# Kernel tuning notes

Hardware: AMD Instinct MI355X
Metric: run time of the kernel (lower is better)

Reference implementation:

```python
import jax, jax.numpy as jnp
import numpy as np

B, NPOS, NNEG, D, NLEM = 8, 512, 512, 128, 32768
MOMENTUM = 0.5
EPS = 1e-12  # F.normalize eps


def setup_inputs() -> dict:
    key = jax.random.key(0)
    k1, k2, k3, k4 = jax.random.split(key, 4)
    x = jax.random.normal(k1, (B, NPOS + NNEG, D), dtype=jnp.float32)
    y = jax.random.randint(k2, (B, NPOS), 0, NPOS).astype(jnp.int64)
    visible = jax.random.randint(k3, (B, NPOS), 0, 2).astype(jnp.int32)
    stdv = 1.0 / np.sqrt(D / 3.0)
    memory = jax.random.uniform(k4, (NLEM, D), dtype=jnp.float32,
                                minval=-stdv, maxval=stdv)
    return {"x": x, "y": y, "visible": visible, "memory": memory, "lru": 3}


def reference(x, y, visible, memory, lru):
    # --- similarity computation (differentiable path) ---
    t = x[:, :NPOS, :]                                  # [B, NPOS, D]
    similarity = jnp.einsum('bpd,md->bpm', t, memory)    # [B, NPOS, NLEM]
    noise_similarity = jnp.einsum('bnd,pd->bnp',
                                  x[:, NPOS:, :], memory[:NPOS])  # [B, NNEG, NPOS]
    y_idx = y.astype(jnp.int64)

    # --- memory bank update (no-grad in original) ---
    vis = visible.astype(x.dtype)[..., None]             # [B, NPOS, 1]
    get = jnp.mean(t * vis, axis=0)                      # [NPOS, D]
    pos_new = memory[:NPOS] * MOMENTUM + get * (1.0 - MOMENTUM)
    neg_flat = x[:, NPOS:, :].reshape(-1, D)             # [B*NNEG, D]
    start = NPOS + lru * NNEG * B                        # lru is a python int
    new_mem = memory.at[start:start + NNEG * B].set(neg_flat)
    new_mem = new_mem.at[:NPOS].set(pos_new)
    norms = jnp.maximum(jnp.linalg.norm(new_mem, axis=1, keepdims=True), EPS)
    new_mem = jax.lax.stop_gradient(new_mem / norms)

    return similarity, y_idx, noise_similarity, new_mem
```

## Files before the change

kernel.cpp:

```cpp
#include <hip/hip_runtime.h>
#include <hip/hip_bf16.h>
#include <cstdint>

#define NPOS 512
#define NNEG 512
#define BATCH 8
#define DDIM 128
#define NLEM 32768
#define NX_ELEM (BATCH * (NPOS + NNEG) * DDIM)
#define NM_ELEM (NLEM * DDIM)
#define NK_STEPS 32

typedef __attribute__((ext_vector_type(4))) float f32x4;
typedef __attribute__((ext_vector_type(16))) float f32x16;
typedef __attribute__((ext_vector_type(8))) short short8;

__device__ __forceinline__ unsigned short f2bf(float f) {
  unsigned u = __float_as_uint(f);
  u = (u + 0x7FFFu + ((u >> 16) & 1u)) >> 16;
  return (unsigned short)u;
}

__device__ __forceinline__ short8 cvt8(f32x4 a0, f32x4 a1) {
  short8 w;
  w[0] = (short)f2bf(a0[0]); w[1] = (short)f2bf(a0[1]);
  w[2] = (short)f2bf(a0[2]); w[3] = (short)f2bf(a0[3]);
  w[4] = (short)f2bf(a1[0]); w[5] = (short)f2bf(a1[1]);
  w[6] = (short)f2bf(a1[2]); w[7] = (short)f2bf(a1[3]);
  return w;
}

__device__ __forceinline__ void async16(const void* g, void* l) {
  __builtin_amdgcn_global_load_lds(
      (const __attribute__((address_space(1))) unsigned int*)g,
      (__attribute__((address_space(3))) unsigned int*)l, 16, 0, 0);
}

__device__ __forceinline__ void newmem_row(int r, int lane, const float* __restrict__ X,
                                           const int* __restrict__ vis,
                                           const float* __restrict__ Mem, int start,
                                           float* __restrict__ out) {
  const int d0 = lane, d1 = lane + 64;
  float v0, v1;
  if (r < NPOS) {
    const float s0 = Mem[(size_t)r * DDIM + d0];
    const float s1 = Mem[(size_t)r * DDIM + d1];
    float a0 = 0.f, a1 = 0.f;
#pragma unroll
    for (int b = 0; b < BATCH; ++b) {
      const float w = (float)vis[b * NPOS + r];
      const float* px = X + (size_t)(b * (NPOS + NNEG) + r) * DDIM;
      a0 += w * px[d0];
      a1 += w * px[d1];
    }
    v0 = 0.5f * s0 + 0.0625f * a0;
    v1 = 0.5f * s1 + 0.0625f * a1;
  } else if (r >= start && r < start + BATCH * NNEG) {
    const int q = r - start;
    const int b = q >> 9, n = q & 511;
    const float* px = X + (size_t)(b * (NPOS + NNEG) + NPOS + n) * DDIM;
    v0 = px[d0];
    v1 = px[d1];
  } else {
    v0 = Mem[(size_t)r * DDIM + d0];
    v1 = Mem[(size_t)r * DDIM + d1];
  }
  float s = v0 * v0 + v1 * v1;
#pragma unroll
  for (int off = 32; off; off >>= 1) s += __shfl_xor(s, off, 64);
  const float inv = 1.0f / fmaxf(sqrtf(s), 1e-12f);
  out[(size_t)r * DDIM + d0] = v0 * inv;
  out[(size_t)r * DDIM + d1] = v1 * inv;
}

__global__ __launch_bounds__(256) void prep_kernel(
    const float* __restrict__ X, const int* __restrict__ y,
    const int* __restrict__ vis, const float* __restrict__ Mem,
    const int* __restrict__ lru_p, unsigned short* __restrict__ xb,
    unsigned short* __restrict__ mb, float* __restrict__ out_y,
    float* __restrict__ out_mem) {
  const int blk = blockIdx.x;
  if (blk < 512) {
    const size_t i = ((size_t)blk * 256 + threadIdx.x) * 8;
    *(short8*)(xb + i) = cvt8(*(const f32x4*)(X + i), *(const f32x4*)(X + i + 4));
  } else if (blk < 2560) {
    const size_t i = ((size_t)(blk - 512) * 256 + threadIdx.x) * 8;
    *(short8*)(mb + i) = cvt8(*(const f32x4*)(Mem + i), *(const f32x4*)(Mem + i + 4));
  } else if (blk < 2576) {
    const int i = (blk - 2560) * 256 + threadIdx.x;
    out_y[i] = (float)y[i];
  } else {
    const int r = (blk - 2576) * 4 + (threadIdx.x >> 6);
    const int start = NPOS + lru_p[0] * (NNEG * BATCH);
    newmem_row(r, threadIdx.x & 63, X, vis, Mem, start, out_mem);
  }
}

__device__ __forceinline__ void hoist_b(const short* Btile, short8 bfr[8][2],
                                        int wc, int la, int lb) {
#pragma unroll
  for (int kk = 0; kk < 8; ++kk)
#pragma unroll
    for (int n2 = 0; n2 < 2; ++n2) {
      const int row = wc * 64 + n2 * 32 + la;
      const int ss = ((kk * 2 + lb) ^ (row & 15)) * 8;
      bfr[kk][n2] = *(const short8*)&Btile[row * 128 + ss];
    }
}

__device__ __forceinline__ void tile_mfma(const short* Atile, const short8 bfr[8][2],
                                          f32x16 acc[2][2], int wr, int la, int lb) {
#pragma unroll
  for (int kk = 0; kk < 8; ++kk) {
    short8 af[2];
#pragma unroll
    for (int m2 = 0; m2 < 2; ++m2) {
      const int row = wr * 64 + m2 * 32 + la;
      const int ss = ((kk * 2 + lb) ^ (row & 15)) * 8;
      af[m2] = *(const short8*)&Atile[row * 128 + ss];
    }
#pragma unroll
    for (int m2 = 0; m2 < 2; ++m2)
#pragma unroll
      for (int n2 = 0; n2 < 2; ++n2)
        acc[m2][n2] = __builtin_amdgcn_mfma_f32_32x32x16_bf16(
            af[m2], bfr[kk][n2], acc[m2][n2], 0, 0, 0);
  }
}

__device__ __forceinline__ void epilogue_store(
    float* __restrict__ ldsC, const f32x16 acc[2][2], float* __restrict__ C,
    int ldc, int m0, int n0c, int t, int wr, int wc, int la, int lb) {
  const int rg = t >> 5, l5 = t & 31;
#pragma unroll
  for (int H = 0; H < 2; ++H) {
    if (wr == H) {
#pragma unroll
      for (int m2 = 0; m2 < 2; ++m2)
#pragma unroll
        for (int n2 = 0; n2 < 2; ++n2) {
          const int colb = wc * 64 + n2 * 32 + la;
          const int rb = m2 * 32 + lb * 4;
#pragma unroll
          for (int r = 0; r < 16; ++r) {
            const int rho = rb + (r & 3) + 8 * (r >> 2);
            ldsC[rho * 132 + colb] = acc[m2][n2][r];
          }
        }
    }
    asm volatile("s_waitcnt lgkmcnt(0)" ::: "memory");
    __builtin_amdgcn_s_barrier();
    __builtin_amdgcn_sched_barrier(0);
#pragma unroll
    for (int i = 0; i < 8; ++i) {
      const int rho = rg + 8 * i;
      const f32x4 v = *(const f32x4*)&ldsC[rho * 132 + l5 * 4];
      *(f32x4*)&C[(size_t)(m0 + H * 64 + rho) * ldc + n0c + l5 * 4] = v;
    }
    if (H == 0) {
      __builtin_amdgcn_s_barrier();
      __builtin_amdgcn_sched_barrier(0);
    }
  }
}

__global__ __launch_bounds__(256, 1) void gemm_band_kernel(
    const unsigned short* __restrict__ Xb, const unsigned short* __restrict__ Mb,
    float* __restrict__ Csim, float* __restrict__ Cnoise) {
  __shared__ short ldsA[2][128 * 128];
  __shared__ short ldsB[128 * 128];
  __shared__ float ldsC[64 * 132];

  const int t = threadIdx.x;
  const int lane = t & 63, wv = t >> 6;
  const int rl = lane >> 4, slot = lane & 15;
  const int wr = wv >> 1, wc = wv & 1;
  const int la = lane & 31, lb = lane >> 5;
  const int b = blockIdx.x;
  const int n0 = b * 128;

  auto stage_tile = [&](short* dst, const unsigned short* src, int rowbase) {
#pragma unroll
    for (int i = 0; i < 8; ++i) {
      const int rowb = wv * 32 + i * 4;
      const int row = rowb + rl;
      const int ss = slot ^ (row & 15);
      async16(src + (size_t)(rowbase + row) * DDIM + ss * 8, &dst[rowb * 128]);
    }
  };

  stage_tile(ldsB, Mb, n0);
  stage_tile(ldsA[0], Xb, 0);
  asm volatile("s_waitcnt vmcnt(0)" ::: "memory");
  __builtin_amdgcn_s_barrier();
  __builtin_amdgcn_sched_barrier(0);

  short8 bfr[8][2];
  hoist_b(ldsB, bfr, wc, la, lb);

  int p = 0;
  for (int k = 0; k < NK_STEPS; ++k) {
    if (k + 1 < NK_STEPS) {
      const int kn = k + 1;
      stage_tile(ldsA[p ^ 1], Xb, (kn >> 2) * 1024 + (kn & 3) * 128);
    } else if (b < 128) {
      const int rp = b >> 2, cb = b & 3;
      stage_tile(ldsA[p ^ 1], Xb, (rp >> 2) * 1024 + 512 + (rp & 3) * 128);
      stage_tile(ldsB, Mb, cb * 128);
    }

    f32x16 acc[2][2] = {};
    tile_mfma(ldsA[p], bfr, acc, wr, la, lb);
    epilogue_store(ldsC, acc, Csim, NLEM, k * 128, n0, t, wr, wc, la, lb);

    if (k + 1 < NK_STEPS || b < 128) {
      asm volatile("s_waitcnt vmcnt(16)" ::: "memory");
      __builtin_amdgcn_s_barrier();
      __builtin_amdgcn_sched_barrier(0);
    }
    p ^= 1;
  }

  if (b < 128) {
    const int rp = b >> 2, cb = b & 3;
    short8 bfr2[8][2];
    hoist_b(ldsB, bfr2, wc, la, lb);
    f32x16 acc[2][2] = {};
    tile_mfma(ldsA[p], bfr2, acc, wr, la, lb);
    epilogue_store(ldsC, acc, Cnoise, NPOS, rp * 128, cb * 128, t, wr, wc, la, lb);
  }
}

__global__ __launch_bounds__(256) void gemm_conv_kernel(
    const float* __restrict__ X, const float* __restrict__ Bm,
    float* __restrict__ C, int ldc, int a_off) {
  __shared__ short lds[2 * 128 * 128];
  short* ldsA = lds;
  short* ldsB = lds + 128 * 128;
  const int t = threadIdx.x;
  const int m0 = blockIdx.x * 128;
  const int n0 = blockIdx.y * 128;
  const int slot = t & 15;
  const int rsub = t >> 4;
#pragma unroll
  for (int it = 0; it < 8; ++it) {
    const int row = it * 16 + rsub;
    const int gr = m0 + row;
    const int xrow = ((gr >> 9) << 10) + (gr & 511) + a_off;
    const f32x4* pa = (const f32x4*)(X + (size_t)xrow * DDIM + slot * 8);
    const f32x4* pb = (const f32x4*)(Bm + (size_t)(n0 + row) * DDIM + slot * 8);
    short8 wa = cvt8(pa[0], pa[1]);
    short8 wb = cvt8(pb[0], pb[1]);
    const int ss = (slot ^ (row & 15)) * 8;
    *(short8*)&ldsA[row * 128 + ss] = wa;
    *(short8*)&ldsB[row * 128 + ss] = wb;
  }
  __syncthreads();
  const int lane = t & 63;
  const int wv = t >> 6;
  const int wr = wv >> 1, wc = wv & 1;
  const int la = lane & 31, lb = lane >> 5;
  short8 bfr[8][2];
  hoist_b(ldsB, bfr, wc, la, lb);
  f32x16 acc[2][2] = {};
  tile_mfma(ldsA, bfr, acc, wr, la, lb);
#pragma unroll
  for (int m2 = 0; m2 < 2; ++m2)
#pragma unroll
    for (int n2 = 0; n2 < 2; ++n2) {
      const int col = n0 + wc * 64 + n2 * 32 + la;
      const int rbase = m0 + wr * 64 + m2 * 32 + lb * 4;
#pragma unroll
      for (int r = 0; r < 16; ++r) {
        const int row = rbase + (r & 3) + 8 * (r >> 2);
        C[(size_t)row * ldc + col] = acc[m2][n2][r];
      }
    }
}

__global__ void y_kernel(const int* __restrict__ y, float* __restrict__ out) {
  const int i = blockIdx.x * blockDim.x + threadIdx.x;
  if (i < BATCH * NPOS) out[i] = (float)y[i];
}

__global__ __launch_bounds__(256) void newmem_kernel(
    const float* __restrict__ X, const int* __restrict__ vis,
    const float* __restrict__ Mem, const int* __restrict__ lru_p,
    float* __restrict__ out) {
  const int r = blockIdx.x * 4 + (threadIdx.x >> 6);
  const int start = NPOS + lru_p[0] * (NNEG * BATCH);
  newmem_row(r, threadIdx.x & 63, X, vis, Mem, start, out);
}

extern "C" void kernel_launch(void* const* d_in, const int* in_sizes, int n_in,
                              void* d_out, int out_size, void* d_ws, size_t ws_size,
                              hipStream_t stream) {
  const float* x = (const float*)d_in[0];
  const int* y = (const int*)d_in[1];
  const int* visible = (const int*)d_in[2];
  const float* memory = (const float*)d_in[3];
  const int* lru = (const int*)d_in[4];
  float* out = (float*)d_out;

  const size_t OFF_Y = (size_t)BATCH * NPOS * NLEM;
  const size_t OFF_NOISE = OFF_Y + (size_t)BATCH * NPOS;
  const size_t OFF_MEM = OFF_NOISE + (size_t)BATCH * NNEG * NPOS;

  const size_t need = (size_t)(NX_ELEM + NM_ELEM) * 2;
  if (ws_size >= need) {
    unsigned short* xb = (unsigned short*)d_ws;
    unsigned short* mb = xb + NX_ELEM;
    prep_kernel<<<10768, 256, 0, stream>>>(
        x, y, visible, memory, lru, xb, mb, out + OFF_Y, out + OFF_MEM);
    gemm_band_kernel<<<256, 256, 0, stream>>>(xb, mb, out, out + OFF_NOISE);
  } else {
    gemm_conv_kernel<<<dim3(32, 256), 256, 0, stream>>>(x, memory, out, NLEM, 0);
    gemm_conv_kernel<<<dim3(32, 4), 256, 0, stream>>>(x, memory, out + OFF_NOISE, NPOS, NPOS);
    y_kernel<<<16, 256, 0, stream>>>(y, out + OFF_Y);
    newmem_kernel<<<NLEM / 4, 256, 0, stream>>>(x, visible, memory, lru, out + OFF_MEM);
  }
}
```

Measured before the change: 143.0 us.

## Split band GEMM across two blocks per band and drop LDS-staged epilogue

The band GEMM now launches 512 blocks instead of 256, with each pair of blocks splitting the 32 row-tile steps of one memory band. The LDS budget shrinks because the B tile reuses the second A buffer and the C staging buffer is removed, which lets two blocks share a CU (launch bounds 2). Results are written straight from the MFMA accumulators, so each store is a scattered 4-byte write rather than a coalesced 16-byte write staged through LDS. The goal is more occupancy and latency hiding, at the cost of less efficient global stores on the large similarity output.

New measurement: 121.1 us, median of 2. 1.18x faster.

```diff
diff --git a/kernel.cpp b/kernel.cpp
--- a/kernel.cpp
+++ b/kernel.cpp
@@ -9,7 +9,6 @@
 #define NLEM 32768
 #define NX_ELEM (BATCH * (NPOS + NNEG) * DDIM)
 #define NM_ELEM (NLEM * DDIM)
-#define NK_STEPS 32
 
 typedef __attribute__((ext_vector_type(4))) float f32x4;
 typedef __attribute__((ext_vector_type(16))) float f32x16;
@@ -128,56 +127,36 @@
   }
 }
 
-__device__ __forceinline__ void epilogue_store(
-    float* __restrict__ ldsC, const f32x16 acc[2][2], float* __restrict__ C,
-    int ldc, int m0, int n0c, int t, int wr, int wc, int la, int lb) {
-  const int rg = t >> 5, l5 = t & 31;
-#pragma unroll
-  for (int H = 0; H < 2; ++H) {
-    if (wr == H) {
-#pragma unroll
-      for (int m2 = 0; m2 < 2; ++m2)
-#pragma unroll
-        for (int n2 = 0; n2 < 2; ++n2) {
-          const int colb = wc * 64 + n2 * 32 + la;
-          const int rb = m2 * 32 + lb * 4;
-#pragma unroll
-          for (int r = 0; r < 16; ++r) {
-            const int rho = rb + (r & 3) + 8 * (r >> 2);
-            ldsC[rho * 132 + colb] = acc[m2][n2][r];
-          }
-        }
-    }
-    asm volatile("s_waitcnt lgkmcnt(0)" ::: "memory");
-    __builtin_amdgcn_s_barrier();
-    __builtin_amdgcn_sched_barrier(0);
-#pragma unroll
-    for (int i = 0; i < 8; ++i) {
-      const int rho = rg + 8 * i;
-      const f32x4 v = *(const f32x4*)&ldsC[rho * 132 + l5 * 4];
-      *(f32x4*)&C[(size_t)(m0 + H * 64 + rho) * ldc + n0c + l5 * 4] = v;
-    }
-    if (H == 0) {
-      __builtin_amdgcn_s_barrier();
-      __builtin_amdgcn_sched_barrier(0);
-    }
-  }
-}
-
-__global__ __launch_bounds__(256, 1) void gemm_band_kernel(
+__device__ __forceinline__ void store_acc(const f32x16 acc[2][2],
+                                          float* __restrict__ C, int ldc, int m0,
+                                          int n0c, int wr, int wc, int la, int lb) {
+#pragma unroll
+  for (int m2 = 0; m2 < 2; ++m2)
+#pragma unroll
+    for (int n2 = 0; n2 < 2; ++n2) {
+      const int col = n0c + wc * 64 + n2 * 32 + la;
+      const int rbase = m0 + wr * 64 + m2 * 32 + lb * 4;
+#pragma unroll
+      for (int r = 0; r < 16; ++r) {
+        const int row = rbase + (r & 3) + 8 * (r >> 2);
+        C[(size_t)row * ldc + col] = acc[m2][n2][r];
+      }
+    }
+}
+
+__global__ __launch_bounds__(256, 2) void gemm_band2_kernel(
     const unsigned short* __restrict__ Xb, const unsigned short* __restrict__ Mb,
     float* __restrict__ Csim, float* __restrict__ Cnoise) {
   __shared__ short ldsA[2][128 * 128];
-  __shared__ short ldsB[128 * 128];
-  __shared__ float ldsC[64 * 132];
 
   const int t = threadIdx.x;
   const int lane = t & 63, wv = t >> 6;
   const int rl = lane >> 4, slot = lane & 15;
   const int wr = wv >> 1, wc = wv & 1;
   const int la = lane & 31, lb = lane >> 5;
-  const int b = blockIdx.x;
-  const int n0 = b * 128;
+  const int blk = blockIdx.x;
+  const int band = blk >> 1, h = blk & 1;
+  const int n0 = band * 128;
 
   auto stage_tile = [&](short* dst, const unsigned short* src, int rowbase) {
 #pragma unroll
@@ -189,45 +168,50 @@
     }
   };
 
-  stage_tile(ldsB, Mb, n0);
-  stage_tile(ldsA[0], Xb, 0);
+  stage_tile(ldsA[1], Mb, n0);
+  {
+    const int K0 = h * 16;
+    stage_tile(ldsA[0], Xb, (K0 >> 2) * 1024 + (K0 & 3) * 128);
+  }
   asm volatile("s_waitcnt vmcnt(0)" ::: "memory");
   __builtin_amdgcn_s_barrier();
   __builtin_amdgcn_sched_barrier(0);
 
   short8 bfr[8][2];
-  hoist_b(ldsB, bfr, wc, la, lb);
+  hoist_b(ldsA[1], bfr, wc, la, lb);
+  asm volatile("s_waitcnt lgkmcnt(0)" ::: "memory");
+  __builtin_amdgcn_s_barrier();
+  __builtin_amdgcn_sched_barrier(0);
 
   int p = 0;
-  for (int k = 0; k < NK_STEPS; ++k) {
-    if (k + 1 < NK_STEPS) {
-      const int kn = k + 1;
-      stage_tile(ldsA[p ^ 1], Xb, (kn >> 2) * 1024 + (kn & 3) * 128);
-    } else if (b < 128) {
-      const int rp = b >> 2, cb = b & 3;
-      stage_tile(ldsA[p ^ 1], Xb, (rp >> 2) * 1024 + 512 + (rp & 3) * 128);
-      stage_tile(ldsB, Mb, cb * 128);
+  for (int k = 0; k < 16; ++k) {
+    if (k + 1 < 16) {
+      const int K = h * 16 + k + 1;
+      stage_tile(ldsA[p ^ 1], Xb, (K >> 2) * 1024 + (K & 3) * 128);
     }
 
     f32x16 acc[2][2] = {};
     tile_mfma(ldsA[p], bfr, acc, wr, la, lb);
-    epilogue_store(ldsC, acc, Csim, NLEM, k * 128, n0, t, wr, wc, la, lb);
-
-    if (k + 1 < NK_STEPS || b < 128) {
-      asm volatile("s_waitcnt vmcnt(16)" ::: "memory");
-      __builtin_amdgcn_s_barrier();
-      __builtin_amdgcn_sched_barrier(0);
-    }
+    store_acc(acc, Csim, NLEM, (h * 16 + k) * 128, n0, wr, wc, la, lb);
+
+    asm volatile("s_waitcnt vmcnt(60)" ::: "memory");
+    __builtin_amdgcn_s_barrier();
+    __builtin_amdgcn_sched_barrier(0);
     p ^= 1;
   }
 
-  if (b < 128) {
-    const int rp = b >> 2, cb = b & 3;
+  if (blk < 128) {
+    const int rp = blk >> 2, cb = blk & 3;
+    stage_tile(ldsA[p ^ 1], Xb, (rp >> 2) * 1024 + 512 + (rp & 3) * 128);
+    stage_tile(ldsA[p], Mb, cb * 128);
+    asm volatile("s_waitcnt vmcnt(0)" ::: "memory");
+    __builtin_amdgcn_s_barrier();
+    __builtin_amdgcn_sched_barrier(0);
     short8 bfr2[8][2];
-    hoist_b(ldsB, bfr2, wc, la, lb);
+    hoist_b(ldsA[p], bfr2, wc, la, lb);
     f32x16 acc[2][2] = {};
-    tile_mfma(ldsA[p], bfr2, acc, wr, la, lb);
-    epilogue_store(ldsC, acc, Cnoise, NPOS, rp * 128, cb * 128, t, wr, wc, la, lb);
+    tile_mfma(ldsA[p ^ 1], bfr2, acc, wr, la, lb);
+    store_acc(acc, Cnoise, NPOS, rp * 128, cb * 128, wr, wc, la, lb);
   }
 }
 
@@ -264,18 +248,7 @@
   hoist_b(ldsB, bfr, wc, la, lb);
   f32x16 acc[2][2] = {};
   tile_mfma(ldsA, bfr, acc, wr, la, lb);
-#pragma unroll
-  for (int m2 = 0; m2 < 2; ++m2)
-#pragma unroll
-    for (int n2 = 0; n2 < 2; ++n2) {
-      const int col = n0 + wc * 64 + n2 * 32 + la;
-      const int rbase = m0 + wr * 64 + m2 * 32 + lb * 4;
-#pragma unroll
-      for (int r = 0; r < 16; ++r) {
-        const int row = rbase + (r & 3) + 8 * (r >> 2);
-        C[(size_t)row * ldc + col] = acc[m2][n2][r];
-      }
-    }
+  store_acc(acc, C, ldc, m0, n0, wr, wc, la, lb);
 }
 
 __global__ void y_kernel(const int* __restrict__ y, float* __restrict__ out) {
@@ -312,7 +285,7 @@
     unsigned short* mb = xb + NX_ELEM;
     prep_kernel<<<10768, 256, 0, stream>>>(
         x, y, visible, memory, lru, xb, mb, out + OFF_Y, out + OFF_MEM);
-    gemm_band_kernel<<<256, 256, 0, stream>>>(xb, mb, out, out + OFF_NOISE);
+    gemm_band2_kernel<<<512, 256, 0, stream>>>(xb, mb, out, out + OFF_NOISE);
   } else {
     gemm_conv_kernel<<<dim3(32, 256), 256, 0, stream>>>(x, memory, out, NLEM, 0);
     gemm_conv_kernel<<<dim3(32, 4), 256, 0, stream>>>(x, memory, out + OFF_NOISE, NPOS, NPOS);
```
